# Kernel optimization log

Measured on AMD Instinct MI355X. Metric: run time of the kernel, lower is better.

## Reference

```python
import jax, jax.numpy as jnp
from jax import lax
import numpy as np

N_SPLITS = 2
N_LEVELS = 3
B, T, C = 32, 1024, 128
HID = 512          # int(input_dim * hidden_size) = 128 * 4
K1, K2 = 5, 3      # first conv kernel_size, second conv kernel=3
N_INTER = 7        # 1 + 2 + 4 interactors in the binary tree
LEAKY_SLOPE = 0.01


def setup_inputs() -> dict:
    key = jax.random.key(0)
    ks = jax.random.split(key, 9)
    w = 0.05  # small init so exp-gating stays well-conditioned
    return {
        "x": jax.random.normal(ks[0], (B, T, C), jnp.float32),
        "mul_w1": jax.random.normal(ks[1], (N_INTER, N_SPLITS, K1, C, HID), jnp.float32) * w,
        "mul_b1": jnp.zeros((N_INTER, N_SPLITS, HID), jnp.float32),
        "mul_w2": jax.random.normal(ks[2], (N_INTER, N_SPLITS, K2, HID, C), jnp.float32) * w,
        "mul_b2": jnp.zeros((N_INTER, N_SPLITS, C), jnp.float32),
        "add_w1": jax.random.normal(ks[3], (N_INTER, N_SPLITS, K1, C, HID), jnp.float32) * w,
        "add_b1": jnp.zeros((N_INTER, N_SPLITS, HID), jnp.float32),
        "add_w2": jax.random.normal(ks[4], (N_INTER, N_SPLITS, K2, HID, C), jnp.float32) * w,
        "add_b2": jnp.zeros((N_INTER, N_SPLITS, C), jnp.float32),
    }


def _leaky(x):
    return jnp.where(x > 0, x, LEAKY_SLOPE * x)


def _causal_conv(x, w, b):
    # x: [B, L, Cin], w: [K, Cin, Cout] (keras WIO layout); 'causal' = left-pad K-1
    k = w.shape[0]
    y = lax.conv_general_dilated(x, w, window_strides=(1,),
                                 padding=[(k - 1, 0)],
                                 dimension_numbers=("NWC", "WIO", "NWC"))
    return y + b


def _conv_seq(x, w1, b1, w2, b2):
    # Conv1D(causal, LeakyReLU 0.01) -> Dropout(identity at inference) -> Conv1D(k=3, causal, tanh)
    h = _leaky(_causal_conv(x, w1, b1))
    return jnp.tanh(_causal_conv(h, w2, b2))


def _interactor(x, idx, p):
    # x: [B, L, C]; strided temporal split into N_SPLITS pieces of length L//N_SPLITS
    splits = [x[:, i::N_SPLITS, :] for i in range(N_SPLITS)]
    scale = N_SPLITS - 1
    mul_list = []
    for i in range(N_SPLITS):
        s = 0.0
        for j in range(N_SPLITS):
            if j != i:
                s = s + _conv_seq(splits[j], p["mul_w1"][idx, i], p["mul_b1"][idx, i],
                                  p["mul_w2"][idx, i], p["mul_b2"][idx, i])
        # prod_j exp(f(x_j)) ** (1/scale) == exp(sum_j f(x_j) / scale)
        mul_list.append(splits[i] * jnp.exp(s / scale))
    out = []
    for i in range(N_SPLITS):
        a = 0.0
        for j in range(N_SPLITS):
            if j != i:
                a = a + _conv_seq(mul_list[j], p["add_w1"][idx, i], p["add_b1"][idx, i],
                                  p["add_w2"][idx, i], p["add_b2"][idx, i])
        a = a / scale
        out.append(mul_list[i] + a if i % 2 == 0 else mul_list[i] - a)
    return out


def reference(x, mul_w1, mul_b1, mul_w2, mul_b2, add_w1, add_b1, add_w2, add_b2):
    p = {"mul_w1": mul_w1, "mul_b1": mul_b1, "mul_w2": mul_w2, "mul_b2": mul_b2,
         "add_w1": add_w1, "add_b1": add_b1, "add_w2": add_w2, "add_b2": add_b2}
    t_in = x.shape[1]
    min_unit = N_SPLITS ** N_LEVELS
    pad = (-t_in) % min_unit  # left zero-pad to a multiple of n_splits**n_levels
    xp = jnp.pad(x, ((0, 0), (pad, 0), (0, 0)))
    seq = [xp]
    idx = 0
    for lvl in range(N_LEVELS):
        nxt = []
        for j in range(N_SPLITS ** lvl):
            nxt += _interactor(seq[j], idx, p)
            idx += 1
        seq = nxt
    # rev_split: recursively concatenate along time with stride `steps`
    while len(seq) > 1:
        steps = len(seq) // N_SPLITS
        seq = [jnp.concatenate([seq[i + s * steps] for s in range(N_SPLITS)], axis=1)
               for i in range(steps)]
    return seq[0][:, -t_in:, :]
```

## Files before the change

kernel.cpp:

```cpp
#include <hip/hip_runtime.h>
#include <hip/hip_bf16.h>
#include <stdint.h>


static constexpr int B_ = 32, T_ = 1024, C_ = 128, HID_ = 512;
static constexpr int K1_ = 5, K2_ = 3;

typedef __attribute__((ext_vector_type(8))) _Float16 half8;
typedef __attribute__((ext_vector_type(4))) float f32x4;

__device__ __forceinline__ unsigned short f2h(float f) {
    _Float16 h = (_Float16)f;
    return __builtin_bit_cast(unsigned short, h);
}

__device__ __forceinline__ void gload16(const void* g, void* l) {
    __builtin_amdgcn_global_load_lds(
        (const __attribute__((address_space(1))) unsigned int*)g,
        (__attribute__((address_space(3))) unsigned int*)l, 16, 0, 0);
}

template<int CIN, int COUT>
__global__ __launch_bounds__(256)
void wprep_k(const float* __restrict__ win1, unsigned short* __restrict__ wout1,
             const float* __restrict__ win2, unsigned short* __restrict__ wout2,
             int nhalf) {
    constexpr int TA = CIN / 64, TB = COUT / 64;
    int blk = blockIdx.x;
    int tb = blk % TB;
    int ta = (blk / TB) % TA;
    int s  = blk / (TA * TB);
    const float* win;
    unsigned short* wout;
    if (s < nhalf) { win = win1; wout = wout1; }
    else           { win = win2; wout = wout2; s -= nhalf; }
    __shared__ float tile[64][65];
    const float* src = win + (size_t)s * CIN * COUT;
    unsigned short* dst = wout + (size_t)s * CIN * COUT;
    int cl = threadIdx.x & 63;
    int rw = threadIdx.x >> 6;
    for (int r = rw; r < 64; r += 4)
        tile[r][cl] = src[(size_t)(ta * 64 + r) * COUT + tb * 64 + cl];
    __syncthreads();
    for (int r = rw; r < 64; r += 4) {
        int co = tb * 64 + r;
        int ci = ta * 64 + cl;
        int ciw = (ci & ~127) | ((ci & 127) ^ ((co & 7) << 3));
        dst[(size_t)co * CIN + ciw] = f2h(tile[cl][r]);
    }
}

__global__ __launch_bounds__(256)
void split_k(const float* __restrict__ cur, unsigned short* __restrict__ outb,
             int Ls) {
    int idx = blockIdx.x * 256 + threadIdx.x;
    int row = idx >> 5;
    int cq  = (idx & 31) << 2;
    int BLs = B_ * Ls;
    int g  = row / BLs;
    int r2 = row - g * BLs;
    int b  = r2 / Ls;
    int u  = r2 - b * Ls;
    int p = g >> 1, i = g & 1;
    const float4 v = *(const float4*)(cur +
        ((size_t)(p * B_ + b) * (2 * Ls) + 2 * u + i) * C_ + cq);
    ushort4 o;
    o.x = f2h(v.x); o.y = f2h(v.y); o.z = f2h(v.z); o.w = f2h(v.w);
    int cqw = cq ^ (((u + 4) & 7) << 3);
    *(ushort4*)(outb + (size_t)row * C_ + cqw) = o;
}

__global__ __launch_bounds__(256, 3)
void conv1_k(const unsigned short* __restrict__ actb,
             const unsigned short* __restrict__ wT,
             const float* __restrict__ bias,
             unsigned short* __restrict__ hid,
             const unsigned short* __restrict__ zp,
             int Ls, int RT, int idxbase) {
    __shared__ unsigned short smemA[132 * 128];
    __shared__ unsigned short smemB[64 * 128];

    const int tid = threadIdx.x;
    const int lane = tid & 63;
    const int w = tid >> 6;
    const int wr = w >> 1, wc = w & 1;

    int blk = blockIdx.x;
    const int ct = blk & 7;
    int t1 = blk >> 3;
    const int rt = t1 % RT;
    const int g  = t1 / RT;
    const int n0 = ct * 64;
    const int rowstart = rt * 128;
    const int b  = rowstart / Ls;
    const int t0 = rowstart - b * Ls;

    const int gin  = g ^ 1;
    const int widx = (idxbase + (g >> 1)) * 2 + (g & 1);

    const char* inb = (const char*)(actb + (size_t)(gin * B_ + b) * Ls * C_);
    const char* wb  = (const char*)(wT + (size_t)widx * (K1_ * HID_ * C_));
    const float* bptr = bias + (size_t)widx * HID_;

    for (int ch = w; ch < 33; ch += 4) {
        int q = ch * 1024 + lane * 16;
        int r = q >> 8;
        int cb = q & 255;
        int t = t0 - 4 + r;
        const char* src = (t >= 0) ? inb + (size_t)t * 256 + cb
                                   : (const char*)zp + cb;
        gload16(src, (char*)smemA + ch * 1024);
    }

    f32x4 acc[4][2];
#pragma unroll
    for (int m = 0; m < 4; ++m)
#pragma unroll
        for (int n = 0; n < 2; ++n) acc[m][n] = (f32x4){0.f, 0.f, 0.f, 0.f};

    for (int kk = 0; kk < K1_; ++kk) {
        if (kk) __syncthreads();
        const char* wt = wb + (size_t)kk * HID_ * C_ * 2;
        for (int ch = w; ch < 16; ch += 4) {
            int q = ch * 1024 + lane * 16;
            int co = q >> 8;
            int cb = q & 255;
            gload16(wt + (size_t)(n0 + co) * 256 + cb, (char*)smemB + ch * 1024);
        }
        asm volatile("s_waitcnt vmcnt(0)" ::: "memory");
        __syncthreads();

#pragma unroll
        for (int ks = 0; ks < 4; ++ks) {
            half8 aF[4], bF[2];
            const int cole = ks * 32 + ((lane >> 4) << 3);
#pragma unroll
            for (int m = 0; m < 4; ++m) {
                int ar = kk + wr * 64 + m * 16 + (lane & 15);
                aF[m] = *(const half8*)(smemA + ar * 128 + (cole ^ ((ar & 7) << 3)));
            }
#pragma unroll
            for (int n = 0; n < 2; ++n) {
                int br = wc * 32 + n * 16 + (lane & 15);
                bF[n] = *(const half8*)(smemB + br * 128 + (cole ^ ((br & 7) << 3)));
            }
#pragma unroll
            for (int m = 0; m < 4; ++m)
#pragma unroll
                for (int n = 0; n < 2; ++n)
                    acc[m][n] = __builtin_amdgcn_mfma_f32_16x16x32_f16(
                        aF[m], bF[n], acc[m][n], 0, 0, 0);
        }
    }

    unsigned short* outp = hid + ((size_t)(g * B_ + b) * Ls + t0) * HID_;
#pragma unroll
    for (int n = 0; n < 2; ++n) {
        int co = n0 + wc * 32 + n * 16 + (lane & 15);
        float bv = bptr[co];
#pragma unroll
        for (int m = 0; m < 4; ++m) {
            int u0 = wr * 64 + m * 16 + ((lane >> 4) << 2);
#pragma unroll
            for (int q = 0; q < 4; ++q) {
                float v = acc[m][n][q] + bv;
                v = (v > 0.f) ? v : 0.01f * v;
                int t = t0 + u0 + q;
                int cow = (co & ~127) | ((co & 127) ^ (((t + 2) & 7) << 3));
                outp[(size_t)(u0 + q) * HID_ + cow] = f2h(v);
            }
        }
    }
}

template<int EPI>
__global__ __launch_bounds__(256, 3)
void conv2_k(const unsigned short* __restrict__ hid,
             const unsigned short* __restrict__ wT,
             const float* __restrict__ bias,
             const float* __restrict__ cur,
             float* __restrict__ mulf,
             unsigned short* __restrict__ actb,
             float* __restrict__ nxt,
             unsigned short* __restrict__ actn,
             float* __restrict__ dout,
             const unsigned short* __restrict__ zp,
             int Ls, int RT, int idxbase) {
    __shared__ unsigned short smemA[66 * 128];
    __shared__ unsigned short smemB[128 * 128];

    const int tid = threadIdx.x;
    const int lane = tid & 63;
    const int w = tid >> 6;
    const int wr = w >> 1, wc = w & 1;

    int blk = blockIdx.x;
    const int rt = blk % RT;
    const int g  = blk / RT;
    const int rowstart = rt * 64;
    const int b  = rowstart / Ls;
    const int t0 = rowstart - b * Ls;
    const int widx = (idxbase + (g >> 1)) * 2 + (g & 1);

    const char* inb = (const char*)(hid + (size_t)(g * B_ + b) * Ls * HID_);
    const char* wb  = (const char*)(wT + (size_t)widx * (K2_ * C_ * HID_));
    const float* bptr = bias + (size_t)widx * C_;

    f32x4 acc[2][4];
#pragma unroll
    for (int m = 0; m < 2; ++m)
#pragma unroll
        for (int n = 0; n < 4; ++n) acc[m][n] = (f32x4){0.f, 0.f, 0.f, 0.f};

    for (int ck = 0; ck < 4; ++ck) {
        if (ck) __syncthreads();
        for (int ch = w; ch < 17; ch += 4) {
            int q = ch * 1024 + lane * 16;
            if (q < 16896) {
                int r = q >> 8;
                int cb = q & 255;
                int t = t0 - 2 + r;
                const char* src = (t >= 0)
                    ? inb + (size_t)t * 1024 + ck * 256 + cb
                    : (const char*)zp + cb;
                gload16(src, (char*)smemA + ch * 1024);
            }
        }
        for (int kk = 0; kk < K2_; ++kk) {
            if (kk) __syncthreads();
            const char* wt = wb + (size_t)kk * C_ * HID_ * 2;
            for (int ch = w; ch < 32; ch += 4) {
                int q = ch * 1024 + lane * 16;
                int co = q >> 8;
                int cb = q & 255;
                gload16(wt + (size_t)co * 1024 + ck * 256 + cb,
                        (char*)smemB + ch * 1024);
            }
            asm volatile("s_waitcnt vmcnt(0)" ::: "memory");
            __syncthreads();

#pragma unroll
            for (int ks = 0; ks < 4; ++ks) {
                half8 aF[2], bF[4];
                const int cole = ks * 32 + ((lane >> 4) << 3);
#pragma unroll
                for (int m = 0; m < 2; ++m) {
                    int ar = kk + wr * 32 + m * 16 + (lane & 15);
                    aF[m] = *(const half8*)(smemA + ar * 128 + (cole ^ ((ar & 7) << 3)));
                }
#pragma unroll
                for (int n = 0; n < 4; ++n) {
                    int br = wc * 64 + n * 16 + (lane & 15);
                    bF[n] = *(const half8*)(smemB + br * 128 + (cole ^ ((br & 7) << 3)));
                }
#pragma unroll
                for (int m = 0; m < 2; ++m)
#pragma unroll
                    for (int n = 0; n < 4; ++n)
                        acc[m][n] = __builtin_amdgcn_mfma_f32_16x16x32_f16(
                            aF[m], bF[n], acc[m][n], 0, 0, 0);
            }
        }
    }

    const size_t rowb = (size_t)(g * B_ + b) * Ls + t0;
    const int p_ = g >> 1, i_ = g & 1;
    const int Ls2 = Ls >> 1;
#pragma unroll
    for (int n = 0; n < 4; ++n) {
        int c = wc * 64 + n * 16 + (lane & 15);
        float bv = bptr[c];
#pragma unroll
        for (int m = 0; m < 2; ++m) {
            int u0 = wr * 32 + m * 16 + ((lane >> 4) << 2);
#pragma unroll
            for (int q = 0; q < 4; ++q) {
                float v = acc[m][n][q] + bv;
                float xc = fminf(fmaxf(v, -15.f), 15.f);
                float e2 = __expf(2.f * xc);
                float th = (e2 - 1.f) / (e2 + 1.f);
                size_t ro = rowb + (size_t)(u0 + q);
                int u = t0 + u0 + q;
                if (EPI == 0) {
                    float sv = cur[((size_t)(p_ * B_ + b) * (2 * Ls) + 2 * u + i_) * C_ + c];
                    float mv = sv * __expf(th);
                    mulf[ro * C_ + c] = mv;
                    int cw = c ^ (((u + 4) & 7) << 3);
                    actb[ro * C_ + cw] = f2h(mv);
                } else {
                    float mv = mulf[ro * C_ + c];
                    float val = (i_ == 0) ? (mv + th) : (mv - th);
                    if (EPI == 1) {
                        nxt[ro * C_ + c] = val;
                        int gq = g * 2 + (u & 1);
                        int uq = u >> 1;
                        int cw = c ^ (((uq + 4) & 7) << 3);
                        actn[((size_t)(gq * B_ + b) * Ls2 + uq) * C_ + cw] = f2h(val);
                    } else {
                        int tau = u | (((g >> 2) & 1) << 7) | (((g >> 1) & 1) << 8)
                                    | ((g & 1) << 9);
                        dout[((size_t)b * T_ + tau) * C_ + c] = val;
                    }
                }
            }
        }
    }
}

extern "C" void kernel_launch(void* const* d_in, const int* in_sizes, int n_in,
                              void* d_out, int out_size, void* d_ws, size_t ws_size,
                              hipStream_t stream) {
    const float* x   = (const float*)d_in[0];
    const float* mw1 = (const float*)d_in[1];
    const float* mb1 = (const float*)d_in[2];
    const float* mw2 = (const float*)d_in[3];
    const float* mb2 = (const float*)d_in[4];
    const float* aw1 = (const float*)d_in[5];
    const float* ab1 = (const float*)d_in[6];
    const float* aw2 = (const float*)d_in[7];
    const float* ab2 = (const float*)d_in[8];

    char* ws = (char*)d_ws;
    size_t off = 0;
    auto alloc = [&](size_t sz) {
        char* p = ws + off;
        off += (sz + 255) & ~(size_t)255;
        return p;
    };
    unsigned short* zp   = (unsigned short*)alloc(8192);
    unsigned short* w1m  = (unsigned short*)alloc((size_t)14 * 5 * 512 * 128 * 2);
    unsigned short* w1a  = (unsigned short*)alloc((size_t)14 * 5 * 512 * 128 * 2);
    unsigned short* w2m  = (unsigned short*)alloc((size_t)14 * 3 * 128 * 512 * 2);
    unsigned short* w2a  = (unsigned short*)alloc((size_t)14 * 3 * 128 * 512 * 2);
    float* bufA          = (float*)alloc((size_t)4194304 * 4);
    float* bufB          = (float*)alloc((size_t)4194304 * 4);
    unsigned short* actb = (unsigned short*)alloc((size_t)4194304 * 2);
    unsigned short* hidb = (unsigned short*)alloc((size_t)16777216 * 2);
    float* mulf          = (float*)alloc((size_t)4194304 * 4);
    (void)ws_size; (void)n_in; (void)in_sizes; (void)out_size;

    hipMemsetAsync(zp, 0, 8192, stream);

    wprep_k<128, 512><<<2240, 256, 0, stream>>>(mw1, w1m, aw1, w1a, 70);
    wprep_k<512, 128><<<1344, 256, 0, stream>>>(mw2, w2m, aw2, w2a, 42);

    split_k<<<4096, 256, 0, stream>>>(x, actb, 512);

    for (int lvl = 0; lvl < 3; ++lvl) {
        const int P = 1 << lvl;
        const int G = 2 * P;
        const int Ls = (1024 >> lvl) >> 1;
        const int idxbase = P - 1;
        const float* cur = (lvl == 0) ? x : ((lvl == 1) ? bufA : bufB);
        float* nxt = (lvl == 1) ? bufB : bufA;
        const int RT1 = Ls / 4;
        const int RT2 = Ls / 2;

        conv1_k<<<G * RT1 * 8, 256, 0, stream>>>(actb, w1m, mb1, hidb, zp,
                                                 Ls, RT1, idxbase);
        conv2_k<0><<<G * RT2, 256, 0, stream>>>(hidb, w2m, mb2, cur, mulf,
                                                actb, nullptr, nullptr, nullptr,
                                                zp, Ls, RT2, idxbase);
        conv1_k<<<G * RT1 * 8, 256, 0, stream>>>(actb, w1a, ab1, hidb, zp,
                                                 Ls, RT1, idxbase);
        if (lvl < 2) {
            conv2_k<1><<<G * RT2, 256, 0, stream>>>(hidb, w2a, ab2, nullptr, mulf,
                                                    nullptr, nxt, actb, nullptr,
                                                    zp, Ls, RT2, idxbase);
        } else {
            conv2_k<2><<<G * RT2, 256, 0, stream>>>(hidb, w2a, ab2, nullptr, mulf,
                                                    nullptr, nullptr, nullptr,
                                                    (float*)d_out,
                                                    zp, Ls, RT2, idxbase);
        }
    }
}
```

Before: 371.9 us.

## Load conv1 weight fragments directly into registers with double-buffered tap prefetch

conv1_k no longer stages weight tiles in shared memory per kernel tap. Each lane loads its B-operand fragments straight from global memory into registers and prefetches the next tap's fragments while the current tap's MFMAs run. This removes four of the five per-tap barriers and the weight LDS traffic, and the conv1 weight prep no longer swizzles since the layout is now read linearly. In exchange it needs more VGPRs for the two fragment buffers, which may hurt occupancy under the 3-blocks launch bound, and each wave reads weights redundantly from global or L2 memory.

```diff
diff --git a/kernel.cpp b/kernel.cpp
--- a/kernel.cpp
+++ b/kernel.cpp
@@ -20,7 +20,7 @@
         (__attribute__((address_space(3))) unsigned int*)l, 16, 0, 0);
 }
 
-template<int CIN, int COUT>
+template<int CIN, int COUT, bool SWZ>
 __global__ __launch_bounds__(256)
 void wprep_k(const float* __restrict__ win1, unsigned short* __restrict__ wout1,
              const float* __restrict__ win2, unsigned short* __restrict__ wout2,
@@ -45,7 +45,7 @@
     for (int r = rw; r < 64; r += 4) {
         int co = tb * 64 + r;
         int ci = ta * 64 + cl;
-        int ciw = (ci & ~127) | ((ci & 127) ^ ((co & 7) << 3));
+        int ciw = SWZ ? ((ci & ~127) | ((ci & 127) ^ ((co & 7) << 3))) : ci;
         dst[(size_t)co * CIN + ciw] = f2h(tile[cl][r]);
     }
 }
@@ -72,13 +72,12 @@
 
 __global__ __launch_bounds__(256, 3)
 void conv1_k(const unsigned short* __restrict__ actb,
-             const unsigned short* __restrict__ wT,
+             const unsigned short* __restrict__ wL,
              const float* __restrict__ bias,
              unsigned short* __restrict__ hid,
              const unsigned short* __restrict__ zp,
              int Ls, int RT, int idxbase) {
     __shared__ unsigned short smemA[132 * 128];
-    __shared__ unsigned short smemB[64 * 128];
 
     const int tid = threadIdx.x;
     const int lane = tid & 63;
@@ -99,8 +98,18 @@
     const int widx = (idxbase + (g >> 1)) * 2 + (g & 1);
 
     const char* inb = (const char*)(actb + (size_t)(gin * B_ + b) * Ls * C_);
-    const char* wb  = (const char*)(wT + (size_t)widx * (K1_ * HID_ * C_));
     const float* bptr = bias + (size_t)widx * HID_;
+
+    const unsigned short* wlane = wL + (size_t)widx * (K1_ * HID_ * C_)
+                                + (size_t)(n0 + wc * 32 + (lane & 15)) * C_
+                                + ((lane >> 4) << 3);
+
+    half8 b0[8], b1[8];
+#pragma unroll
+    for (int n = 0; n < 2; ++n)
+#pragma unroll
+        for (int ks = 0; ks < 4; ++ks)
+            b0[n * 4 + ks] = *(const half8*)(wlane + (size_t)n * 16 * C_ + ks * 32);
 
     for (int ch = w; ch < 33; ch += 4) {
         int q = ch * 1024 + lane * 16;
@@ -111,6 +120,8 @@
                                    : (const char*)zp + cb;
         gload16(src, (char*)smemA + ch * 1024);
     }
+    asm volatile("s_waitcnt vmcnt(0)" ::: "memory");
+    __syncthreads();
 
     f32x4 acc[4][2];
 #pragma unroll
@@ -118,21 +129,18 @@
 #pragma unroll
         for (int n = 0; n < 2; ++n) acc[m][n] = (f32x4){0.f, 0.f, 0.f, 0.f};
 
-    for (int kk = 0; kk < K1_; ++kk) {
-        if (kk) __syncthreads();
-        const char* wt = wb + (size_t)kk * HID_ * C_ * 2;
-        for (int ch = w; ch < 16; ch += 4) {
-            int q = ch * 1024 + lane * 16;
-            int co = q >> 8;
-            int cb = q & 255;
-            gload16(wt + (size_t)(n0 + co) * 256 + cb, (char*)smemB + ch * 1024);
-        }
-        asm volatile("s_waitcnt vmcnt(0)" ::: "memory");
-        __syncthreads();
-
+    auto tap = [&](const int kk, half8 (&bc)[8], half8 (&bn)[8]) {
+        if (kk < K1_ - 1) {
+            const unsigned short* wn = wlane + (size_t)(kk + 1) * HID_ * C_;
+#pragma unroll
+            for (int n = 0; n < 2; ++n)
+#pragma unroll
+                for (int ks = 0; ks < 4; ++ks)
+                    bn[n * 4 + ks] = *(const half8*)(wn + (size_t)n * 16 * C_ + ks * 32);
+        }
 #pragma unroll
         for (int ks = 0; ks < 4; ++ks) {
-            half8 aF[4], bF[2];
+            half8 aF[4];
             const int cole = ks * 32 + ((lane >> 4) << 3);
 #pragma unroll
             for (int m = 0; m < 4; ++m) {
@@ -140,18 +148,19 @@
                 aF[m] = *(const half8*)(smemA + ar * 128 + (cole ^ ((ar & 7) << 3)));
             }
 #pragma unroll
-            for (int n = 0; n < 2; ++n) {
-                int br = wc * 32 + n * 16 + (lane & 15);
-                bF[n] = *(const half8*)(smemB + br * 128 + (cole ^ ((br & 7) << 3)));
-            }
-#pragma unroll
-            for (int m = 0; m < 4; ++m)
-#pragma unroll
-                for (int n = 0; n < 2; ++n)
-                    acc[m][n] = __builtin_amdgcn_mfma_f32_16x16x32_f16(
-                        aF[m], bF[n], acc[m][n], 0, 0, 0);
-        }
-    }
+            for (int m = 0; m < 4; ++m) {
+                acc[m][0] = __builtin_amdgcn_mfma_f32_16x16x32_f16(
+                    aF[m], bc[ks], acc[m][0], 0, 0, 0);
+                acc[m][1] = __builtin_amdgcn_mfma_f32_16x16x32_f16(
+                    aF[m], bc[4 + ks], acc[m][1], 0, 0, 0);
+            }
+        }
+    };
+    tap(0, b0, b1);
+    tap(1, b1, b0);
+    tap(2, b0, b1);
+    tap(3, b1, b0);
+    tap(4, b0, b1);
 
     unsigned short* outp = hid + ((size_t)(g * B_ + b) * Ls + t0) * HID_;
 #pragma unroll
@@ -341,8 +350,8 @@
 
     hipMemsetAsync(zp, 0, 8192, stream);
 
-    wprep_k<128, 512><<<2240, 256, 0, stream>>>(mw1, w1m, aw1, w1a, 70);
-    wprep_k<512, 128><<<1344, 256, 0, stream>>>(mw2, w2m, aw2, w2a, 42);
+    wprep_k<128, 512, false><<<2240, 256, 0, stream>>>(mw1, w1m, aw1, w1a, 70);
+    wprep_k<512, 128, true ><<<1344, 256, 0, stream>>>(mw2, w2m, aw2, w2a, 42);
 
     split_k<<<4096, 256, 0, stream>>>(x, actb, 512);
 
```

Measured after the change: 472.1 us. 1.27x slower.
